# Kernel optimization log

Hardware: AMD Instinct MI355X
Metric: run time of the kernel (lower is better)

Reference implementation:

```python
import jax, jax.numpy as jnp
import numpy as np

B, C, G, E, R, T, L, K = 8, 192, 256, 384, 4, 8192, 3, 3
DILATIONS = (1, 3, 9)
EPS = 1e-5


def setup_inputs() -> dict:
    key = jax.random.key(0)
    ks = jax.random.split(key, 16)
    s = 0.05
    return {
        'x': jax.random.normal(ks[0], (B, C, T), jnp.float32),
        'x_mask': jnp.ones((B, 1, T), jnp.float32),
        'g': jax.random.normal(ks[1], (B, G, 1), jnp.float32),
        'dconv_w': jax.random.normal(ks[2], (L, C, K), jnp.float32) * s,
        'dconv_b': jax.random.normal(ks[3], (L, C), jnp.float32) * s,
        'ln_gamma': jnp.ones((L, C), jnp.float32),
        'ln_beta': jnp.zeros((L, C), jnp.float32),
        'p1_w': jax.random.normal(ks[4], (L, E, C), jnp.float32) * s,
        'p1_b': jax.random.normal(ks[5], (L, E), jnp.float32) * s,
        'p1_ain_w': jax.random.normal(ks[6], (L, C * R, G), jnp.float32) * 0.01,
        'p1_ain_b': jnp.zeros((L, C * R), jnp.float32),
        'p1_aout_w': jax.random.normal(ks[7], (L, E * R, G), jnp.float32) * 0.01,
        'p1_aout_b': jnp.zeros((L, E * R), jnp.float32),
        'p2_w': jax.random.normal(ks[8], (L, C, E), jnp.float32) * s,
        'p2_b': jax.random.normal(ks[9], (L, C), jnp.float32) * s,
        'p2_ain_w': jax.random.normal(ks[10], (L, E * R, G), jnp.float32) * 0.01,
        'p2_ain_b': jnp.zeros((L, E * R), jnp.float32),
        'p2_aout_w': jax.random.normal(ks[11], (L, C * R, G), jnp.float32) * 0.01,
        'p2_aout_b': jnp.zeros((L, C * R), jnp.float32),
    }


def _causal_dconv(x, w, b, dilation):
    # x: [B,C,T]; w: [C,K] depthwise kernel; matches flip/pad/conv/flip in torch module
    xf = jnp.flip(x, 2)
    xf = jnp.pad(xf, ((0, 0), (0, 0), (0, (K - 1) * dilation)))
    y = jax.lax.conv_general_dilated(
        xf, w[:, None, :], window_strides=(1,), padding='VALID',
        rhs_dilation=(dilation,), dimension_numbers=('NCH', 'OIH', 'NCH'),
        feature_group_count=C)
    y = y + b[None, :, None]
    return jnp.flip(y, 2)


def _layernorm_c(x, gamma, beta):
    # LayerNorm over channel axis (axis=1)
    mu = jnp.mean(x, axis=1, keepdims=True)
    var = jnp.mean(jnp.square(x - mu), axis=1, keepdims=True)
    xn = (x - mu) * jax.lax.rsqrt(var + EPS)
    return xn * gamma[None, :, None] + beta[None, :, None]


def _lora(x, g2, w_main, b_main, ain_w, ain_b, aout_w, aout_b, cin, cout):
    # main 1x1 conv
    x_ = jnp.einsum('oc,bcl->bol', w_main, x) + b_main[None, :, None]
    a_in = (g2 @ ain_w.T + ain_b).reshape(-1, cin, R)      # [B,cin,R]
    a_out = (g2 @ aout_w.T + aout_b).reshape(-1, R, cout)  # [B,R,cout]
    t = jnp.einsum('bcl,bcr->brl', x, a_in)
    low = jnp.einsum('brl,brc->bcl', t, a_out)
    return x_ + low


def reference(x, x_mask, g, dconv_w, dconv_b, ln_gamma, ln_beta,
              p1_w, p1_b, p1_ain_w, p1_ain_b, p1_aout_w, p1_aout_b,
              p2_w, p2_b, p2_ain_w, p2_ain_b, p2_aout_w, p2_aout_b):
    g2 = g[:, :, 0]  # [B,G]
    x = x * x_mask
    for i in range(L):
        residual = x
        h = _causal_dconv(x, dconv_w[i], dconv_b[i], DILATIONS[i])
        h = _layernorm_c(h, ln_gamma[i], ln_beta[i])
        h = h * x_mask
        h = _lora(h, g2, p1_w[i], p1_b[i], p1_ain_w[i], p1_ain_b[i],
                  p1_aout_w[i], p1_aout_b[i], C, E)
        h = jax.nn.gelu(h, approximate=False)
        h = _lora(h, g2, p2_w[i], p2_b[i], p2_ain_w[i], p2_ain_b[i],
                  p2_aout_w[i], p2_aout_b[i], E, C)
        x = residual + h
    return x
```

## Files before the change

### kernel.cpp

```cpp
#include <hip/hip_runtime.h>
#include <hip/hip_bf16.h>

#define B_ 8
#define C_ 192
#define G_ 256
#define E_ 384
#define R_ 4
#define T_ 8192
#define L_ 3
#define K_ 3

typedef __attribute__((ext_vector_type(4))) float f32x4;
typedef __attribute__((ext_vector_type(8))) short bf16x8;
typedef __attribute__((ext_vector_type(4))) short bf16x4;

static __device__ __forceinline__ float bf2f(short u) {
    union { float f; unsigned int i; } z;
    z.i = ((unsigned int)(unsigned short)u) << 16;
    return z.f;
}

static __device__ __forceinline__ float gelu_fast(float x) {
    float x2 = x * x;
    float inner = fmaf(0.044715f * x, x2, x);
    float e = __expf(1.5957691216057308f * inner);
    float r = 1.0f / (e + 1.0f);
    float t = fmaf(-2.0f, r, 1.0f);
    float s = 0.5f * x;
    return fmaf(s, t, s);
}

__global__ __launch_bounds__(256) void adapters_kernel(
    const float* __restrict__ g2,
    const float* __restrict__ w0, const float* __restrict__ bi0, float* __restrict__ o0,
    const float* __restrict__ w1, const float* __restrict__ bi1, float* __restrict__ o1,
    const float* __restrict__ w2, const float* __restrict__ bi2, float* __restrict__ o2,
    const float* __restrict__ w3, const float* __restrict__ bi3, float* __restrict__ o3)
{
    const int N0 = L_ * B_ * (C_ * R_);
    const int N1 = L_ * B_ * (E_ * R_);
    int idx = blockIdx.x * 256 + threadIdx.x;
    const float* w; const float* bi; float* o; int rows; int li;
    if (idx < N0)                      { w=w0; bi=bi0; o=o0; rows=C_*R_; li=idx; }
    else if ((idx -= N0) < N1)         { w=w1; bi=bi1; o=o1; rows=E_*R_; li=idx; }
    else if ((idx -= N1) < N1)         { w=w2; bi=bi2; o=o2; rows=E_*R_; li=idx; }
    else if ((idx -= N1) < N0)         { w=w3; bi=bi3; o=o3; rows=C_*R_; li=idx; }
    else return;
    int bb = li & 7;
    int lr = li >> 3;
    const float4* wr = (const float4*)(w + (size_t)lr * G_);
    const float4* gb = (const float4*)(g2 + (size_t)bb * G_);
    float s = bi[lr];
#pragma unroll 8
    for (int g = 0; g < G_ / 4; ++g) {
        float4 a = gb[g], b = wr[g];
        s = fmaf(a.x, b.x, s); s = fmaf(a.y, b.y, s);
        s = fmaf(a.z, b.z, s); s = fmaf(a.w, b.w, s);
    }
    o[((size_t)(lr / rows) * B_ + bb) * rows + (lr % rows)] = s;
}

__global__ __launch_bounds__(256) void builds_kernel(
    const float* __restrict__ p1w, const float* __restrict__ p2w,
    const float* __restrict__ A1in, const float* __restrict__ A1out,
    const float* __restrict__ A2in, const float* __restrict__ A2out,
    __hip_bfloat16* __restrict__ W1, __hip_bfloat16* __restrict__ W2)
{
    const int W1B = (L_ * B_ * E_ * C_) / 256;
    int blk = blockIdx.x;
    if (blk < W1B) {
        int idx = blk * 256 + threadIdx.x;
        int c = idx % C_;
        int e = (idx / C_) % E_;
        int b = (idx / (C_ * E_)) % B_;
        int l = idx / (C_ * E_ * B_);
        float v = p1w[((size_t)l * E_ + e) * C_ + c];
        const float* ai = A1in + ((size_t)l * B_ + b) * (C_ * R_);
        const float* ao = A1out + ((size_t)l * B_ + b) * (R_ * E_);
#pragma unroll
        for (int r = 0; r < R_; ++r) v = fmaf(ai[c * R_ + r], ao[r * E_ + e], v);
        W1[idx] = __float2bfloat16(v);
    } else {
        int idx = (blk - W1B) * 256 + threadIdx.x;
        int e = idx % E_;
        int c = (idx / E_) % C_;
        int b = (idx / (C_ * E_)) % B_;
        int l = idx / (C_ * E_ * B_);
        float v = p2w[((size_t)l * C_ + c) * E_ + e];
        const float* ai = A2in + ((size_t)l * B_ + b) * (E_ * R_);
        const float* ao = A2out + ((size_t)l * B_ + b) * (R_ * C_);
#pragma unroll
        for (int r = 0; r < R_; ++r) v = fmaf(ai[e * R_ + r], ao[r * C_ + c], v);
        W2[idx] = __float2bfloat16(v);
    }
}

__global__ __launch_bounds__(256) void transpose_in_kernel(
    const float* __restrict__ x, const float* __restrict__ mask,
    __hip_bfloat16* __restrict__ xw)
{
    __shared__ float tile[64][65];
    int b = blockIdx.z, c0 = blockIdx.y * 64, t0 = blockIdx.x * 64;
#pragma unroll
    for (int it = 0; it < 4; ++it) {
        int i = it * 256 + threadIdx.x;
        int r = i >> 4, cq = i & 15;
        float4 xv = *(const float4*)(&x[((size_t)b * C_ + c0 + r) * T_ + t0 + cq * 4]);
        float4 mv = *(const float4*)(&mask[(size_t)b * T_ + t0 + cq * 4]);
        tile[r][cq * 4 + 0] = xv.x * mv.x;
        tile[r][cq * 4 + 1] = xv.y * mv.y;
        tile[r][cq * 4 + 2] = xv.z * mv.z;
        tile[r][cq * 4 + 3] = xv.w * mv.w;
    }
    __syncthreads();
#pragma unroll
    for (int it = 0; it < 4; ++it) {
        int i = it * 256 + threadIdx.x;
        int r = i >> 4, cq = i & 15;
        union { __hip_bfloat16 h[4]; int2 i2; } u;
#pragma unroll
        for (int j = 0; j < 4; ++j) u.h[j] = __float2bfloat16(tile[cq * 4 + j][r]);
        *(int2*)(&xw[((size_t)b * T_ + t0 + r) * C_ + c0 + cq * 4]) = u.i2;
    }
}

struct StageRegs { bf16x4 xv[4][3][3]; };

static __device__ __forceinline__ void stage_load(
    const __hip_bfloat16* __restrict__ xin, size_t xbase,
    int t0s, int dil, int grp, int cbase, StageRegs& sr)
{
#pragma unroll
    for (int rr = 0; rr < 4; ++rr) {
        int t = t0s + grp * 4 + rr;
#pragma unroll
        for (int k3 = 0; k3 < 3; ++k3) {
            int tt = t - k3 * dil;
            bool ok = (tt >= 0);
            const __hip_bfloat16* rp =
                xin + xbase + (size_t)(ok ? tt : 0) * C_ + cbase;
#pragma unroll
            for (int q = 0; q < 3; ++q) {
                bf16x4 z = *(const bf16x4*)(rp + q * 4);
                if (!ok) z = (bf16x4){0, 0, 0, 0};
                sr.xv[rr][k3][q] = z;
            }
        }
    }
}

static __device__ __forceinline__ void stage_compute(
    const StageRegs& sr,
    const float* __restrict__ dw, const float* __restrict__ db,
    const float* __restrict__ gamma, const float* __restrict__ beta,
    const float* __restrict__ mask,
    int b, int t0s, int grp, int cbase,
    __hip_bfloat16 (* __restrict__ Hst)[C_ + 8])
{
    float4 wf[9], dbf[3], gaf[3], bef[3];
#pragma unroll
    for (int q = 0; q < 9; ++q) wf[q] = *(const float4*)(dw + cbase * 3 + q * 4);
#pragma unroll
    for (int q = 0; q < 3; ++q) {
        dbf[q] = *(const float4*)(db + cbase + q * 4);
        gaf[q] = *(const float4*)(gamma + cbase + q * 4);
        bef[q] = *(const float4*)(beta + cbase + q * 4);
    }
#pragma unroll
    for (int rr = 0; rr < 4; ++rr) {
        int tl = grp * 4 + rr;
        int t = t0s + tl;
        float v[12];
#pragma unroll
        for (int j = 0; j < 12; ++j) v[j] = ((const float*)dbf)[j];
#pragma unroll
        for (int k3 = 0; k3 < 3; ++k3)
#pragma unroll
            for (int q = 0; q < 3; ++q)
#pragma unroll
                for (int jj = 0; jj < 4; ++jj) {
                    int j = q * 4 + jj;
                    v[j] = fmaf(((const float*)wf)[j * 3 + k3],
                                bf2f(sr.xv[rr][k3][q][jj]), v[j]);
                }
        float s = 0.f, sq = 0.f;
#pragma unroll
        for (int j = 0; j < 12; ++j) { s += v[j]; sq = fmaf(v[j], v[j], sq); }
#pragma unroll
        for (int o = 1; o <= 8; o <<= 1) {
            s += __shfl_xor(s, o, 64);
            sq += __shfl_xor(sq, o, 64);
        }
        float mu = s * (1.f / C_);
        float var = fmaf(sq, 1.f / C_, -mu * mu);
        float rs = rsqrtf(var + 1e-5f);
        float m = mask[(size_t)b * T_ + t];
        union { __hip_bfloat16 h[12]; int2 i2[3]; } u;
#pragma unroll
        for (int j = 0; j < 12; ++j) {
            float xn = (v[j] - mu) * rs;
            u.h[j] = __float2bfloat16(
                fmaf(xn, ((const float*)gaf)[j], ((const float*)bef)[j]) * m);
        }
#pragma unroll
        for (int q = 0; q < 3; ++q)
            *(int2*)(&Hst[tl][cbase + q * 4]) = u.i2[q];
    }
}

template<int NT, bool LAST>
__global__ __launch_bounds__(256, 2) void ffn_fused_kernel(
    const __hip_bfloat16* __restrict__ xin, __hip_bfloat16* __restrict__ xout,
    const float* __restrict__ dw, const float* __restrict__ db,
    const float* __restrict__ gamma, const float* __restrict__ beta,
    const float* __restrict__ mask,
    const __hip_bfloat16* __restrict__ W1, const float* __restrict__ b1,
    const __hip_bfloat16* __restrict__ W2, const float* __restrict__ b2,
    int dil, float* __restrict__ outF)
{
    __shared__ __align__(16) char smem[75776];
    __hip_bfloat16 (*Hs)[C_ + 8]  = (__hip_bfloat16 (*)[C_ + 8])smem;
    __hip_bfloat16 (*H1s)[E_ + 8] = (__hip_bfloat16 (*)[E_ + 8])(smem + 25600);

    const int bid = blockIdx.x;
    const int b = bid & 7;
    const int tbase = (bid >> 3) * 64 * NT;
    const int tid = threadIdx.x;
    const int wv = tid >> 6, lane = tid & 63;
    const int llo = lane & 15, lhi = lane >> 4;
    const int grp = tid >> 4, cbase = (tid & 15) * 12;
    const size_t xbase = (size_t)b * T_ * C_;
    const __hip_bfloat16* W1b = W1 + (size_t)b * E_ * C_;
    const __hip_bfloat16* W2b = W2 + (size_t)b * C_ * E_;

    StageRegs sr;
    stage_load(xin, xbase, tbase, dil, grp, cbase, sr);
    stage_compute(sr, dw, db, gamma, beta, mask, b, tbase, grp, cbase, Hs);
    __syncthreads();

#pragma unroll
    for (int it = 0; it < NT; ++it) {
        const int t0 = tbase + it * 64;

        if (it + 1 < NT)
            stage_load(xin, xbase, t0 + 64, dil, grp, cbase, sr);

        const __hip_bfloat16* w1p = W1b + (size_t)(wv * 96 + llo) * C_ + lhi * 8;
        f32x4 acc1[6][4] = {};
#pragma unroll
        for (int kc = 0; kc < 6; ++kc) {
            bf16x8 bfr[4];
#pragma unroll
            for (int nf = 0; nf < 4; ++nf)
                bfr[nf] = *(const bf16x8*)(&Hs[nf * 16 + llo][kc * 32 + lhi * 8]);
#pragma unroll
            for (int mf = 0; mf < 6; ++mf) {
                bf16x8 af = *(const bf16x8*)(w1p + (size_t)mf * 16 * C_ + kc * 32);
#pragma unroll
                for (int nf = 0; nf < 4; ++nf)
                    acc1[mf][nf] = __builtin_amdgcn_mfma_f32_16x16x32_bf16(
                        af, bfr[nf], acc1[mf][nf], 0, 0, 0);
            }
        }

#pragma unroll
        for (int mf = 0; mf < 6; ++mf) {
            int e0 = wv * 96 + mf * 16 + lhi * 4;
            float4 b1v = *(const float4*)(b1 + e0);
#pragma unroll
            for (int nf = 0; nf < 4; ++nf) {
                union { __hip_bfloat16 h[4]; int2 i2; } u;
#pragma unroll
                for (int j = 0; j < 4; ++j) {
                    float xx = acc1[mf][nf][j] + ((const float*)&b1v)[j];
                    u.h[j] = __float2bfloat16(gelu_fast(xx));
                }
                *(int2*)(&H1s[nf * 16 + llo][e0]) = u.i2;
            }
        }
        __syncthreads();

        const __hip_bfloat16* w2p = W2b + (size_t)(wv * 48 + llo) * E_ + lhi * 8;
        f32x4 acc2[3][4] = {};
#pragma unroll
        for (int kc = 0; kc < 12; ++kc) {
            bf16x8 bfr[4];
#pragma unroll
            for (int nf = 0; nf < 4; ++nf)
                bfr[nf] = *(const bf16x8*)(&H1s[nf * 16 + llo][kc * 32 + lhi * 8]);
#pragma unroll
            for (int mf = 0; mf < 3; ++mf) {
                bf16x8 af = *(const bf16x8*)(w2p + (size_t)mf * 16 * E_ + kc * 32);
#pragma unroll
                for (int nf = 0; nf < 4; ++nf)
                    acc2[mf][nf] = __builtin_amdgcn_mfma_f32_16x16x32_bf16(
                        af, bfr[nf], acc2[mf][nf], 0, 0, 0);
            }
        }

        if (!LAST) {
#pragma unroll
            for (int mf = 0; mf < 3; ++mf) {
                int c0 = wv * 48 + mf * 16 + lhi * 4;
                float4 b2v = *(const float4*)(b2 + c0);
#pragma unroll
                for (int nf = 0; nf < 4; ++nf) {
                    int t = t0 + nf * 16 + llo;
                    const __hip_bfloat16* pr = xin + xbase + (size_t)t * C_ + c0;
                    __hip_bfloat16* po = xout + xbase + (size_t)t * C_ + c0;
                    union { __hip_bfloat16 h[4]; int2 i2; } ui, uo;
                    ui.i2 = *(const int2*)pr;
#pragma unroll
                    for (int j = 0; j < 4; ++j)
                        uo.h[j] = __float2bfloat16(
                            bf2f(*(short*)&ui.h[j]) + acc2[mf][nf][j] + ((const float*)&b2v)[j]);
                    *(int2*)po = uo.i2;
                }
            }
            if (it + 1 < NT) {
                stage_compute(sr, dw, db, gamma, beta, mask, b, t0 + 64, grp, cbase, Hs);
                __syncthreads();
            }
        } else {
            float (*Tile)[68] = (float (*)[68])smem;
            __syncthreads();
#pragma unroll
            for (int mf = 0; mf < 3; ++mf) {
                int c0 = wv * 48 + mf * 16 + lhi * 4;
                float4 b2v = *(const float4*)(b2 + c0);
#pragma unroll
                for (int nf = 0; nf < 4; ++nf) {
                    int tl = nf * 16 + llo;
                    const __hip_bfloat16* pr = xin + xbase + (size_t)(t0 + tl) * C_ + c0;
                    union { __hip_bfloat16 h[4]; int2 i2; } ui;
                    ui.i2 = *(const int2*)pr;
#pragma unroll
                    for (int j = 0; j < 4; ++j)
                        Tile[c0 + j][tl] =
                            bf2f(*(short*)&ui.h[j]) + acc2[mf][nf][j] + ((const float*)&b2v)[j];
                }
            }
            __syncthreads();
#pragma unroll
            for (int it2 = 0; it2 < 12; ++it2) {
                int i = it2 * 256 + tid;
                int r = i >> 4, tq = i & 15;
                float4 o = *(const float4*)(&Tile[r][tq * 4]);
                *(float4*)(&outF[((size_t)b * C_ + r) * T_ + t0 + tq * 4]) = o;
            }
        }
    }
}

extern "C" void kernel_launch(void* const* d_in, const int* in_sizes, int n_in,
                              void* d_out, int out_size, void* d_ws, size_t ws_size,
                              hipStream_t stream) {
    const float* x        = (const float*)d_in[0];
    const float* x_mask   = (const float*)d_in[1];
    const float* g        = (const float*)d_in[2];
    const float* dconv_w  = (const float*)d_in[3];
    const float* dconv_b  = (const float*)d_in[4];
    const float* ln_gamma = (const float*)d_in[5];
    const float* ln_beta  = (const float*)d_in[6];
    const float* p1_w     = (const float*)d_in[7];
    const float* p1_b     = (const float*)d_in[8];
    const float* p1_ain_w = (const float*)d_in[9];
    const float* p1_ain_b = (const float*)d_in[10];
    const float* p1_aout_w= (const float*)d_in[11];
    const float* p1_aout_b= (const float*)d_in[12];
    const float* p2_w     = (const float*)d_in[13];
    const float* p2_b     = (const float*)d_in[14];
    const float* p2_ain_w = (const float*)d_in[15];
    const float* p2_ain_b = (const float*)d_in[16];
    const float* p2_aout_w= (const float*)d_in[17];
    const float* p2_aout_b= (const float*)d_in[18];

    char* ws = (char*)d_ws;
    size_t off = 0;
    __hip_bfloat16* xwA = (__hip_bfloat16*)(ws + off); off += (size_t)B_ * T_ * C_ * 2;
    __hip_bfloat16* xwB = (__hip_bfloat16*)(ws + off); off += (size_t)B_ * T_ * C_ * 2;
    __hip_bfloat16* W1 = (__hip_bfloat16*)(ws + off);  off += (size_t)L_ * B_ * E_ * C_ * 2;
    __hip_bfloat16* W2 = (__hip_bfloat16*)(ws + off);  off += (size_t)L_ * B_ * C_ * E_ * 2;
    float* A1in  = (float*)(ws + off); off += (size_t)L_ * B_ * C_ * R_ * 4;
    float* A1out = (float*)(ws + off); off += (size_t)L_ * B_ * R_ * E_ * 4;
    float* A2in  = (float*)(ws + off); off += (size_t)L_ * B_ * E_ * R_ * 4;
    float* A2out = (float*)(ws + off); off += (size_t)L_ * B_ * R_ * C_ * 4;

    {
        int total = L_ * B_ * (2 * C_ * R_ + 2 * E_ * R_);
        adapters_kernel<<<(total + 255) / 256, 256, 0, stream>>>(
            g,
            p1_ain_w, p1_ain_b, A1in,
            p1_aout_w, p1_aout_b, A1out,
            p2_ain_w, p2_ain_b, A2in,
            p2_aout_w, p2_aout_b, A2out);
    }
    {
        int w1blocks = (L_ * B_ * E_ * C_) / 256;
        builds_kernel<<<2 * w1blocks, 256, 0, stream>>>(
            p1_w, p2_w, A1in, A1out, A2in, A2out, W1, W2);
    }

    transpose_in_kernel<<<dim3(T_ / 64, C_ / 64, B_), 256, 0, stream>>>(x, x_mask, xwA);

    const int DILS[3] = {1, 3, 9};
    __hip_bfloat16* bufs[2] = {xwA, xwB};
    for (int l = 0; l < L_; ++l) {
        if (l < L_ - 1) {
            ffn_fused_kernel<2, false><<<(T_ / 128) * B_, 256, 0, stream>>>(
                bufs[l & 1], bufs[(l & 1) ^ 1],
                dconv_w + l * C_ * K_, dconv_b + l * C_,
                ln_gamma + l * C_, ln_beta + l * C_, x_mask,
                W1 + (size_t)l * B_ * E_ * C_, p1_b + l * E_,
                W2 + (size_t)l * B_ * C_ * E_, p2_b + l * C_, DILS[l], nullptr);
        } else {
            ffn_fused_kernel<1, true><<<(T_ / 64) * B_, 256, 0, stream>>>(
                bufs[l & 1], bufs[(l & 1) ^ 1],
                dconv_w + l * C_ * K_, dconv_b + l * C_,
                ln_gamma + l * C_, ln_beta + l * C_, x_mask,
                W1 + (size_t)l * B_ * E_ * C_, p1_b + l * E_,
                W2 + (size_t)l * B_ * C_ * E_, p2_b + l * C_, DILS[l], (float*)d_out);
        }
    }
}
```

Before: 228.0 us.

## Split first two layers into dconv/LN, GEMM1+GELU, and GEMM2+residual kernels

For the first two layers, the fused per-layer FFN kernel is replaced by three kernels: depthwise conv plus layernorm written to a bf16 buffer, an LDS-tiled GEMM1 with GELU writing H1 (the output buffer reused as scratch), and an LDS-tiled GEMM2 with the residual add. The last layer keeps the fused kernel. The goal is better GEMM tiling, weight reuse and occupancy than the fused kernel, which read weights straight from global memory. The cost is extra global traffic for the H and H1 intermediates plus more kernel launches.

New measurement: 244.9 us. +7.4%, slower.

```diff
diff --git a/kernel.cpp b/kernel.cpp
--- a/kernel.cpp
+++ b/kernel.cpp
@@ -18,6 +18,11 @@
     union { float f; unsigned int i; } z;
     z.i = ((unsigned int)(unsigned short)u) << 16;
     return z.f;
+}
+
+static __device__ __forceinline__ short f2bf(float f) {
+    __hip_bfloat16 h = __float2bfloat16(f);
+    return *(short*)&h;
 }
 
 static __device__ __forceinline__ float gelu_fast(float x) {
@@ -208,6 +213,253 @@
     }
 }
 
+__global__ __launch_bounds__(256) void dconv_ln_kernel(
+    const __hip_bfloat16* __restrict__ xin, __hip_bfloat16* __restrict__ Hout,
+    const float* __restrict__ dw, const float* __restrict__ db,
+    const float* __restrict__ gamma, const float* __restrict__ beta,
+    const float* __restrict__ mask, int dil)
+{
+    const int b = blockIdx.y;
+    const int t0 = blockIdx.x * 64;
+    const int tid = threadIdx.x;
+    const int grp = tid >> 4, cbase = (tid & 15) * 12;
+    const size_t xbase = (size_t)b * T_ * C_;
+
+    StageRegs sr;
+    stage_load(xin, xbase, t0, dil, grp, cbase, sr);
+
+    float4 wf[9], dbf[3], gaf[3], bef[3];
+#pragma unroll
+    for (int q = 0; q < 9; ++q) wf[q] = *(const float4*)(dw + cbase * 3 + q * 4);
+#pragma unroll
+    for (int q = 0; q < 3; ++q) {
+        dbf[q] = *(const float4*)(db + cbase + q * 4);
+        gaf[q] = *(const float4*)(gamma + cbase + q * 4);
+        bef[q] = *(const float4*)(beta + cbase + q * 4);
+    }
+#pragma unroll
+    for (int rr = 0; rr < 4; ++rr) {
+        int tl = grp * 4 + rr;
+        int t = t0 + tl;
+        float v[12];
+#pragma unroll
+        for (int j = 0; j < 12; ++j) v[j] = ((const float*)dbf)[j];
+#pragma unroll
+        for (int k3 = 0; k3 < 3; ++k3)
+#pragma unroll
+            for (int q = 0; q < 3; ++q)
+#pragma unroll
+                for (int jj = 0; jj < 4; ++jj) {
+                    int j = q * 4 + jj;
+                    v[j] = fmaf(((const float*)wf)[j * 3 + k3],
+                                bf2f(sr.xv[rr][k3][q][jj]), v[j]);
+                }
+        float s = 0.f, sq = 0.f;
+#pragma unroll
+        for (int j = 0; j < 12; ++j) { s += v[j]; sq = fmaf(v[j], v[j], sq); }
+#pragma unroll
+        for (int o = 1; o <= 8; o <<= 1) {
+            s += __shfl_xor(s, o, 64);
+            sq += __shfl_xor(sq, o, 64);
+        }
+        float mu = s * (1.f / C_);
+        float var = fmaf(sq, 1.f / C_, -mu * mu);
+        float rs = rsqrtf(var + 1e-5f);
+        float m = mask[(size_t)b * T_ + t];
+        union { __hip_bfloat16 h[12]; int2 i2[3]; } u;
+#pragma unroll
+        for (int j = 0; j < 12; ++j) {
+            float xn = (v[j] - mu) * rs;
+            u.h[j] = __float2bfloat16(
+                fmaf(xn, ((const float*)gaf)[j], ((const float*)bef)[j]) * m);
+        }
+        __hip_bfloat16* orow = Hout + xbase + (size_t)t * C_ + cbase;
+#pragma unroll
+        for (int q = 0; q < 3; ++q)
+            *(int2*)(orow + q * 4) = u.i2[q];
+    }
+}
+
+__global__ __launch_bounds__(256, 3) void gemm1_kernel(
+    const __hip_bfloat16* __restrict__ H,
+    const __hip_bfloat16* __restrict__ W1, const float* __restrict__ b1,
+    __hip_bfloat16* __restrict__ H1)
+{
+    __shared__ __align__(16) char smem[46080];
+    __hip_bfloat16 (*As)[72] = (__hip_bfloat16(*)[72])smem;
+    __hip_bfloat16 (*Bs)[72] = (__hip_bfloat16(*)[72])(smem + 27648);
+    __hip_bfloat16 (*Tile)[104] = (__hip_bfloat16(*)[104])smem;
+
+    const int bid = blockIdx.x;
+    const int b = bid & 7;
+    const int rest = bid >> 3;
+    const int mt = rest & 1;
+    const int nt = rest >> 1;
+    const int m0 = mt * 192;
+    const int t0 = nt * 128;
+    const int tid = threadIdx.x;
+    const int wv = tid >> 6, lane = tid & 63;
+    const int wm = wv >> 1, wn = wv & 1;
+    const int llo = lane & 15, lhi = lane >> 4;
+    const int srow = tid >> 3, scol = (tid & 7) * 8;
+    const __hip_bfloat16* Wb = W1 + (size_t)b * E_ * C_;
+    const __hip_bfloat16* Hb = H + (size_t)b * T_ * C_;
+
+    f32x4 acc[6][4] = {};
+#pragma unroll
+    for (int kk = 0; kk < 3; ++kk) {
+        if (kk) __syncthreads();
+#pragma unroll
+        for (int p = 0; p < 6; ++p) {
+            int r = p * 32 + srow;
+            *(bf16x8*)(&As[r][scol]) =
+                *(const bf16x8*)(&Wb[(size_t)(m0 + r) * C_ + kk * 64 + scol]);
+        }
+#pragma unroll
+        for (int p = 0; p < 4; ++p) {
+            int r = p * 32 + srow;
+            *(bf16x8*)(&Bs[r][scol]) =
+                *(const bf16x8*)(&Hb[(size_t)(t0 + r) * C_ + kk * 64 + scol]);
+        }
+        __syncthreads();
+#pragma unroll
+        for (int kc = 0; kc < 2; ++kc) {
+            bf16x8 bfr[4];
+#pragma unroll
+            for (int nf = 0; nf < 4; ++nf)
+                bfr[nf] = *(const bf16x8*)(&Bs[wn * 64 + nf * 16 + llo][kc * 32 + lhi * 8]);
+#pragma unroll
+            for (int mf = 0; mf < 6; ++mf) {
+                bf16x8 af = *(const bf16x8*)(&As[wm * 96 + mf * 16 + llo][kc * 32 + lhi * 8]);
+#pragma unroll
+                for (int nf = 0; nf < 4; ++nf)
+                    acc[mf][nf] = __builtin_amdgcn_mfma_f32_16x16x32_bf16(
+                        af, bfr[nf], acc[mf][nf], 0, 0, 0);
+            }
+        }
+    }
+
+#pragma unroll
+    for (int h = 0; h < 2; ++h) {
+        __syncthreads();
+        if (wm == h) {
+#pragma unroll
+            for (int mf = 0; mf < 6; ++mf) {
+                int e0 = m0 + h * 96 + mf * 16 + lhi * 4;
+                float4 b1v = *(const float4*)(b1 + e0);
+#pragma unroll
+                for (int nf = 0; nf < 4; ++nf) {
+                    union { __hip_bfloat16 x[4]; int2 i2; } u;
+#pragma unroll
+                    for (int j = 0; j < 4; ++j)
+                        u.x[j] = __float2bfloat16(
+                            gelu_fast(acc[mf][nf][j] + ((const float*)&b1v)[j]));
+                    *(int2*)(&Tile[wn * 64 + nf * 16 + llo][mf * 16 + lhi * 4]) = u.i2;
+                }
+            }
+        }
+        __syncthreads();
+#pragma unroll
+        for (int i = 0; i < 6; ++i) {
+            int idx = i * 256 + tid;
+            int r = idx / 12, c16 = idx % 12;
+            bf16x8 v = *(const bf16x8*)(&Tile[r][c16 * 8]);
+            *(bf16x8*)(&H1[((size_t)b * T_ + t0 + r) * E_ + m0 + h * 96 + c16 * 8]) = v;
+        }
+    }
+}
+
+__global__ __launch_bounds__(256, 3) void gemm2_kernel(
+    const __hip_bfloat16* __restrict__ H1,
+    const __hip_bfloat16* __restrict__ W2, const float* __restrict__ b2,
+    const __hip_bfloat16* __restrict__ xin, __hip_bfloat16* __restrict__ xout)
+{
+    __shared__ __align__(16) char smem[46080];
+    __hip_bfloat16 (*As)[72] = (__hip_bfloat16(*)[72])smem;
+    __hip_bfloat16 (*Bs)[72] = (__hip_bfloat16(*)[72])(smem + 27648);
+    __hip_bfloat16 (*Tile)[104] = (__hip_bfloat16(*)[104])smem;
+
+    const int bid = blockIdx.x;
+    const int b = bid & 7;
+    const int nt = bid >> 3;
+    const int t0 = nt * 128;
+    const int tid = threadIdx.x;
+    const int wv = tid >> 6, lane = tid & 63;
+    const int wm = wv >> 1, wn = wv & 1;
+    const int llo = lane & 15, lhi = lane >> 4;
+    const int srow = tid >> 3, scol = (tid & 7) * 8;
+    const __hip_bfloat16* Wb = W2 + (size_t)b * C_ * E_;
+    const __hip_bfloat16* H1b = H1 + (size_t)b * T_ * E_;
+
+    f32x4 acc[6][4] = {};
+#pragma unroll
+    for (int kk = 0; kk < 6; ++kk) {
+        if (kk) __syncthreads();
+#pragma unroll
+        for (int p = 0; p < 6; ++p) {
+            int r = p * 32 + srow;
+            *(bf16x8*)(&As[r][scol]) =
+                *(const bf16x8*)(&Wb[(size_t)r * E_ + kk * 64 + scol]);
+        }
+#pragma unroll
+        for (int p = 0; p < 4; ++p) {
+            int r = p * 32 + srow;
+            *(bf16x8*)(&Bs[r][scol]) =
+                *(const bf16x8*)(&H1b[(size_t)(t0 + r) * E_ + kk * 64 + scol]);
+        }
+        __syncthreads();
+#pragma unroll
+        for (int kc = 0; kc < 2; ++kc) {
+            bf16x8 bfr[4];
+#pragma unroll
+            for (int nf = 0; nf < 4; ++nf)
+                bfr[nf] = *(const bf16x8*)(&Bs[wn * 64 + nf * 16 + llo][kc * 32 + lhi * 8]);
+#pragma unroll
+            for (int mf = 0; mf < 6; ++mf) {
+                bf16x8 af = *(const bf16x8*)(&As[wm * 96 + mf * 16 + llo][kc * 32 + lhi * 8]);
+#pragma unroll
+                for (int nf = 0; nf < 4; ++nf)
+                    acc[mf][nf] = __builtin_amdgcn_mfma_f32_16x16x32_bf16(
+                        af, bfr[nf], acc[mf][nf], 0, 0, 0);
+            }
+        }
+    }
+
+#pragma unroll
+    for (int h = 0; h < 2; ++h) {
+        __syncthreads();
+        if (wm == h) {
+#pragma unroll
+            for (int mf = 0; mf < 6; ++mf) {
+                int c0 = h * 96 + mf * 16 + lhi * 4;
+                float4 b2v = *(const float4*)(b2 + c0);
+#pragma unroll
+                for (int nf = 0; nf < 4; ++nf) {
+                    union { __hip_bfloat16 x[4]; int2 i2; } u;
+#pragma unroll
+                    for (int j = 0; j < 4; ++j)
+                        u.x[j] = __float2bfloat16(acc[mf][nf][j] + ((const float*)&b2v)[j]);
+                    *(int2*)(&Tile[wn * 64 + nf * 16 + llo][mf * 16 + lhi * 4]) = u.i2;
+                }
+            }
+        }
+        __syncthreads();
+#pragma unroll
+        for (int i = 0; i < 6; ++i) {
+            int idx = i * 256 + tid;
+            int r = idx / 12, c16 = idx % 12;
+            bf16x8 tv = *(const bf16x8*)(&Tile[r][c16 * 8]);
+            size_t goff = ((size_t)b * T_ + t0 + r) * C_ + h * 96 + c16 * 8;
+            bf16x8 rv = *(const bf16x8*)(&xin[goff]);
+            union { short s[8]; bf16x8 v; } ov;
+#pragma unroll
+            for (int j = 0; j < 8; ++j)
+                ov.s[j] = f2bf(bf2f(tv[j]) + bf2f(rv[j]));
+            *(bf16x8*)(&xout[goff]) = ov.v;
+        }
+    }
+}
+
 template<int NT, bool LAST>
 __global__ __launch_bounds__(256, 2) void ffn_fused_kernel(
     const __hip_bfloat16* __restrict__ xin, __hip_bfloat16* __restrict__ xout,
@@ -241,7 +493,6 @@
 #pragma unroll
     for (int it = 0; it < NT; ++it) {
         const int t0 = tbase + it * 64;
-
         if (it + 1 < NT)
             stage_load(xin, xbase, t0 + 64, dil, grp, cbase, sr);
 
@@ -262,7 +513,6 @@
                         af, bfr[nf], acc1[mf][nf], 0, 0, 0);
             }
         }
-
 #pragma unroll
         for (int mf = 0; mf < 6; ++mf) {
             int e0 = wv * 96 + mf * 16 + lhi * 4;
@@ -377,14 +627,17 @@
 
     char* ws = (char*)d_ws;
     size_t off = 0;
-    __hip_bfloat16* xwA = (__hip_bfloat16*)(ws + off); off += (size_t)B_ * T_ * C_ * 2;
-    __hip_bfloat16* xwB = (__hip_bfloat16*)(ws + off); off += (size_t)B_ * T_ * C_ * 2;
-    __hip_bfloat16* W1 = (__hip_bfloat16*)(ws + off);  off += (size_t)L_ * B_ * E_ * C_ * 2;
-    __hip_bfloat16* W2 = (__hip_bfloat16*)(ws + off);  off += (size_t)L_ * B_ * C_ * E_ * 2;
+    __hip_bfloat16* P0 = (__hip_bfloat16*)(ws + off); off += (size_t)B_ * T_ * C_ * 2;
+    __hip_bfloat16* P1 = (__hip_bfloat16*)(ws + off); off += (size_t)B_ * T_ * C_ * 2;
+    __hip_bfloat16* P2 = (__hip_bfloat16*)(ws + off); off += (size_t)B_ * T_ * C_ * 2;
+    __hip_bfloat16* W1 = (__hip_bfloat16*)(ws + off); off += (size_t)L_ * B_ * E_ * C_ * 2;
+    __hip_bfloat16* W2 = (__hip_bfloat16*)(ws + off); off += (size_t)L_ * B_ * C_ * E_ * 2;
     float* A1in  = (float*)(ws + off); off += (size_t)L_ * B_ * C_ * R_ * 4;
     float* A1out = (float*)(ws + off); off += (size_t)L_ * B_ * R_ * E_ * 4;
     float* A2in  = (float*)(ws + off); off += (size_t)L_ * B_ * E_ * R_ * 4;
     float* A2out = (float*)(ws + off); off += (size_t)L_ * B_ * R_ * C_ * 4;
+
+    __hip_bfloat16* H1 = (__hip_bfloat16*)d_out;
 
     {
         int total = L_ * B_ * (2 * C_ * R_ + 2 * E_ * R_);
@@ -401,25 +654,26 @@
             p1_w, p2_w, A1in, A1out, A2in, A2out, W1, W2);
     }
 
-    transpose_in_kernel<<<dim3(T_ / 64, C_ / 64, B_), 256, 0, stream>>>(x, x_mask, xwA);
+    transpose_in_kernel<<<dim3(T_ / 64, C_ / 64, B_), 256, 0, stream>>>(x, x_mask, P0);
 
     const int DILS[3] = {1, 3, 9};
-    __hip_bfloat16* bufs[2] = {xwA, xwB};
-    for (int l = 0; l < L_; ++l) {
-        if (l < L_ - 1) {
-            ffn_fused_kernel<2, false><<<(T_ / 128) * B_, 256, 0, stream>>>(
-                bufs[l & 1], bufs[(l & 1) ^ 1],
-                dconv_w + l * C_ * K_, dconv_b + l * C_,
-                ln_gamma + l * C_, ln_beta + l * C_, x_mask,
-                W1 + (size_t)l * B_ * E_ * C_, p1_b + l * E_,
-                W2 + (size_t)l * B_ * C_ * E_, p2_b + l * C_, DILS[l], nullptr);
-        } else {
-            ffn_fused_kernel<1, true><<<(T_ / 64) * B_, 256, 0, stream>>>(
-                bufs[l & 1], bufs[(l & 1) ^ 1],
-                dconv_w + l * C_ * K_, dconv_b + l * C_,
-                ln_gamma + l * C_, ln_beta + l * C_, x_mask,
-                W1 + (size_t)l * B_ * E_ * C_, p1_b + l * E_,
-                W2 + (size_t)l * B_ * C_ * E_, p2_b + l * C_, DILS[l], (float*)d_out);
-        }
-    }
-}
+    __hip_bfloat16* INS[2]  = {P0, P2};
+    __hip_bfloat16* HBS[2]  = {P1, P0};
+    __hip_bfloat16* OUTS[2] = {P2, P1};
+    for (int l = 0; l < 2; ++l) {
+        dconv_ln_kernel<<<dim3(T_ / 64, B_), 256, 0, stream>>>(
+            INS[l], HBS[l],
+            dconv_w + l * C_ * K_, dconv_b + l * C_,
+            ln_gamma + l * C_, ln_beta + l * C_, x_mask, DILS[l]);
+        gemm1_kernel<<<(E_ / 192) * (T_ / 128) * B_, 256, 0, stream>>>(
+            HBS[l], W1 + (size_t)l * B_ * E_ * C_, p1_b + l * E_, H1);
+        gemm2_kernel<<<(T_ / 128) * B_, 256, 0, stream>>>(
+            H1, W2 + (size_t)l * B_ * C_ * E_, p2_b + l * C_, INS[l], OUTS[l]);
+    }
+    ffn_fused_kernel<1, true><<<(T_ / 64) * B_, 256, 0, stream>>>(
+        P1, (__hip_bfloat16*)nullptr,
+        dconv_w + 2 * C_ * K_, dconv_b + 2 * C_,
+        ln_gamma + 2 * C_, ln_beta + 2 * C_, x_mask,
+        W1 + (size_t)2 * B_ * E_ * C_, p1_b + 2 * E_,
+        W2 + (size_t)2 * B_ * C_ * E_, p2_b + 2 * C_, DILS[2], (float*)d_out);
+}
```

## Switch fused FFN GEMMs to 32x32x16 MFMA with 2x2 wave tiling for GEMM2

Applied to the files above, without the earlier changes.

Both pointwise-conv GEMMs now use the 32x32x16 bf16 MFMA instead of 16x16x32, and the epilogue index mapping is rewritten for the 32x32 accumulator layout. The second GEMM splits the four waves 2x2 over channels and time rather than only over channels, and LDS row strides are padded to +10 elements. The aim is fewer MFMA issues and fewer LDS B-fragment reads per FLOP, plus less bank conflicting. The cost is a changed register footprint and a possible LDS alignment issue, since the odd padding breaks 16-byte alignment of the bf16x8 reads.

After: 281.7 us. +23.6%, slower.

```diff
diff --git a/kernel.cpp b/kernel.cpp
--- a/kernel.cpp
+++ b/kernel.cpp
@@ -11,8 +11,12 @@
 #define K_ 3
 
 typedef __attribute__((ext_vector_type(4))) float f32x4;
+typedef __attribute__((ext_vector_type(16))) float f32x16;
 typedef __attribute__((ext_vector_type(8))) short bf16x8;
 typedef __attribute__((ext_vector_type(4))) short bf16x4;
+
+#define HS_STRIDE  (C_ + 10)
+#define H1S_STRIDE (E_ + 10)
 
 static __device__ __forceinline__ float bf2f(short u) {
     union { float f; unsigned int i; } z;
@@ -155,7 +159,7 @@
     const float* __restrict__ gamma, const float* __restrict__ beta,
     const float* __restrict__ mask,
     int b, int t0s, int grp, int cbase,
-    __hip_bfloat16 (* __restrict__ Hst)[C_ + 8])
+    __hip_bfloat16 (* __restrict__ Hst)[HS_STRIDE])
 {
     float4 wf[9], dbf[3], gaf[3], bef[3];
 #pragma unroll
@@ -218,16 +222,17 @@
     const __hip_bfloat16* __restrict__ W2, const float* __restrict__ b2,
     int dil, float* __restrict__ outF)
 {
-    __shared__ __align__(16) char smem[75776];
-    __hip_bfloat16 (*Hs)[C_ + 8]  = (__hip_bfloat16 (*)[C_ + 8])smem;
-    __hip_bfloat16 (*H1s)[E_ + 8] = (__hip_bfloat16 (*)[E_ + 8])(smem + 25600);
+    __shared__ __align__(16) char smem[76288];
+    __hip_bfloat16 (*Hs)[HS_STRIDE]  = (__hip_bfloat16 (*)[HS_STRIDE])smem;
+    __hip_bfloat16 (*H1s)[H1S_STRIDE] =
+        (__hip_bfloat16 (*)[H1S_STRIDE])(smem + 25856);
 
     const int bid = blockIdx.x;
     const int b = bid & 7;
     const int tbase = (bid >> 3) * 64 * NT;
     const int tid = threadIdx.x;
     const int wv = tid >> 6, lane = tid & 63;
-    const int llo = lane & 15, lhi = lane >> 4;
+    const int l31 = lane & 31, khalf = lane >> 5;
     const int grp = tid >> 4, cbase = (tid & 15) * 12;
     const size_t xbase = (size_t)b * T_ * C_;
     const __hip_bfloat16* W1b = W1 + (size_t)b * E_ * C_;
@@ -245,78 +250,78 @@
         if (it + 1 < NT)
             stage_load(xin, xbase, t0 + 64, dil, grp, cbase, sr);
 
-        const __hip_bfloat16* w1p = W1b + (size_t)(wv * 96 + llo) * C_ + lhi * 8;
-        f32x4 acc1[6][4] = {};
-#pragma unroll
-        for (int kc = 0; kc < 6; ++kc) {
-            bf16x8 bfr[4];
-#pragma unroll
-            for (int nf = 0; nf < 4; ++nf)
-                bfr[nf] = *(const bf16x8*)(&Hs[nf * 16 + llo][kc * 32 + lhi * 8]);
-#pragma unroll
-            for (int mf = 0; mf < 6; ++mf) {
-                bf16x8 af = *(const bf16x8*)(w1p + (size_t)mf * 16 * C_ + kc * 32);
-#pragma unroll
-                for (int nf = 0; nf < 4; ++nf)
-                    acc1[mf][nf] = __builtin_amdgcn_mfma_f32_16x16x32_bf16(
-                        af, bfr[nf], acc1[mf][nf], 0, 0, 0);
-            }
-        }
-
-#pragma unroll
-        for (int mf = 0; mf < 6; ++mf) {
-            int e0 = wv * 96 + mf * 16 + lhi * 4;
-            float4 b1v = *(const float4*)(b1 + e0);
-#pragma unroll
-            for (int nf = 0; nf < 4; ++nf) {
-                union { __hip_bfloat16 h[4]; int2 i2; } u;
-#pragma unroll
-                for (int j = 0; j < 4; ++j) {
-                    float xx = acc1[mf][nf][j] + ((const float*)&b1v)[j];
-                    u.h[j] = __float2bfloat16(gelu_fast(xx));
+        const __hip_bfloat16* w1p =
+            W1b + (size_t)(wv * 96 + l31) * C_ + khalf * 8;
+        f32x16 acc1[3][2] = {};
+#pragma unroll
+        for (int kk = 0; kk < 12; ++kk) {
+            bf16x8 bfr[2];
+#pragma unroll
+            for (int nt2 = 0; nt2 < 2; ++nt2)
+                bfr[nt2] = *(const bf16x8*)(&Hs[nt2 * 32 + l31][kk * 16 + khalf * 8]);
+#pragma unroll
+            for (int mt = 0; mt < 3; ++mt) {
+                bf16x8 af = *(const bf16x8*)(w1p + (size_t)mt * 32 * C_ + kk * 16);
+#pragma unroll
+                for (int nt2 = 0; nt2 < 2; ++nt2)
+                    acc1[mt][nt2] = __builtin_amdgcn_mfma_f32_32x32x16_bf16(
+                        af, bfr[nt2], acc1[mt][nt2], 0, 0, 0);
+            }
+        }
+
+#pragma unroll
+        for (int mt = 0; mt < 3; ++mt)
+#pragma unroll
+            for (int nt2 = 0; nt2 < 2; ++nt2) {
+                int trow = nt2 * 32 + l31;
+#pragma unroll
+                for (int q = 0; q < 4; ++q) {
+                    int e0 = wv * 96 + mt * 32 + khalf * 4 + q * 8;
+                    float4 b1v = *(const float4*)(b1 + e0);
+                    union { __hip_bfloat16 h[4]; int2 i2; } u;
+#pragma unroll
+                    for (int r = 0; r < 4; ++r)
+                        u.h[r] = __float2bfloat16(gelu_fast(
+                            acc1[mt][nt2][4 * q + r] + ((const float*)&b1v)[r]));
+                    *(int2*)(&H1s[trow][e0]) = u.i2;
                 }
-                *(int2*)(&H1s[nf * 16 + llo][e0]) = u.i2;
-            }
-        }
+            }
         __syncthreads();
 
-        const __hip_bfloat16* w2p = W2b + (size_t)(wv * 48 + llo) * E_ + lhi * 8;
-        f32x4 acc2[3][4] = {};
-#pragma unroll
-        for (int kc = 0; kc < 12; ++kc) {
-            bf16x8 bfr[4];
-#pragma unroll
-            for (int nf = 0; nf < 4; ++nf)
-                bfr[nf] = *(const bf16x8*)(&H1s[nf * 16 + llo][kc * 32 + lhi * 8]);
-#pragma unroll
-            for (int mf = 0; mf < 3; ++mf) {
-                bf16x8 af = *(const bf16x8*)(w2p + (size_t)mf * 16 * E_ + kc * 32);
-#pragma unroll
-                for (int nf = 0; nf < 4; ++nf)
-                    acc2[mf][nf] = __builtin_amdgcn_mfma_f32_16x16x32_bf16(
-                        af, bfr[nf], acc2[mf][nf], 0, 0, 0);
+        const int wm = wv >> 1, wn = wv & 1;
+        const __hip_bfloat16* w2p =
+            W2b + (size_t)(wm * 96 + l31) * E_ + khalf * 8;
+        f32x16 acc2[3] = {};
+#pragma unroll
+        for (int kk = 0; kk < 24; ++kk) {
+            bf16x8 bfr = *(const bf16x8*)(&H1s[wn * 32 + l31][kk * 16 + khalf * 8]);
+#pragma unroll
+            for (int mt = 0; mt < 3; ++mt) {
+                bf16x8 af = *(const bf16x8*)(w2p + (size_t)mt * 32 * E_ + kk * 16);
+                acc2[mt] = __builtin_amdgcn_mfma_f32_32x32x16_bf16(
+                    af, bfr, acc2[mt], 0, 0, 0);
             }
         }
 
         if (!LAST) {
-#pragma unroll
-            for (int mf = 0; mf < 3; ++mf) {
-                int c0 = wv * 48 + mf * 16 + lhi * 4;
-                float4 b2v = *(const float4*)(b2 + c0);
-#pragma unroll
-                for (int nf = 0; nf < 4; ++nf) {
-                    int t = t0 + nf * 16 + llo;
-                    const __hip_bfloat16* pr = xin + xbase + (size_t)t * C_ + c0;
-                    __hip_bfloat16* po = xout + xbase + (size_t)t * C_ + c0;
+            int t = t0 + wn * 32 + l31;
+            const __hip_bfloat16* pr = xin + xbase + (size_t)t * C_;
+            __hip_bfloat16* po = xout + xbase + (size_t)t * C_;
+#pragma unroll
+            for (int mt = 0; mt < 3; ++mt)
+#pragma unroll
+                for (int q = 0; q < 4; ++q) {
+                    int c0 = wm * 96 + mt * 32 + khalf * 4 + q * 8;
+                    float4 b2v = *(const float4*)(b2 + c0);
                     union { __hip_bfloat16 h[4]; int2 i2; } ui, uo;
-                    ui.i2 = *(const int2*)pr;
-#pragma unroll
-                    for (int j = 0; j < 4; ++j)
-                        uo.h[j] = __float2bfloat16(
-                            bf2f(*(short*)&ui.h[j]) + acc2[mf][nf][j] + ((const float*)&b2v)[j]);
-                    *(int2*)po = uo.i2;
+                    ui.i2 = *(const int2*)(pr + c0);
+#pragma unroll
+                    for (int r = 0; r < 4; ++r)
+                        uo.h[r] = __float2bfloat16(
+                            bf2f(*(short*)&ui.h[r]) + acc2[mt][4 * q + r]
+                            + ((const float*)&b2v)[r]);
+                    *(int2*)(po + c0) = uo.i2;
                 }
-            }
             if (it + 1 < NT) {
                 stage_compute(sr, dw, db, gamma, beta, mask, b, t0 + 64, grp, cbase, Hs);
                 __syncthreads();
@@ -324,21 +329,23 @@
         } else {
             float (*Tile)[68] = (float (*)[68])smem;
             __syncthreads();
-#pragma unroll
-            for (int mf = 0; mf < 3; ++mf) {
-                int c0 = wv * 48 + mf * 16 + lhi * 4;
-                float4 b2v = *(const float4*)(b2 + c0);
-#pragma unroll
-                for (int nf = 0; nf < 4; ++nf) {
-                    int tl = nf * 16 + llo;
-                    const __hip_bfloat16* pr = xin + xbase + (size_t)(t0 + tl) * C_ + c0;
-                    union { __hip_bfloat16 h[4]; int2 i2; } ui;
-                    ui.i2 = *(const int2*)pr;
-#pragma unroll
-                    for (int j = 0; j < 4; ++j)
-                        Tile[c0 + j][tl] =
-                            bf2f(*(short*)&ui.h[j]) + acc2[mf][nf][j] + ((const float*)&b2v)[j];
-                }
+            {
+                int tl = wn * 32 + l31;
+                const __hip_bfloat16* pr = xin + xbase + (size_t)(t0 + tl) * C_;
+#pragma unroll
+                for (int mt = 0; mt < 3; ++mt)
+#pragma unroll
+                    for (int q = 0; q < 4; ++q) {
+                        int c0 = wm * 96 + mt * 32 + khalf * 4 + q * 8;
+                        float4 b2v = *(const float4*)(b2 + c0);
+                        union { __hip_bfloat16 h[4]; int2 i2; } ui;
+                        ui.i2 = *(const int2*)(pr + c0);
+#pragma unroll
+                        for (int r = 0; r < 4; ++r)
+                            Tile[c0 + r][tl] =
+                                bf2f(*(short*)&ui.h[r]) + acc2[mt][4 * q + r]
+                                + ((const float*)&b2v)[r];
+                    }
             }
             __syncthreads();
 #pragma unroll
```
